# Kernel optimization log

Measured on AMD Instinct MI355X. Metric: run time of the kernel, lower is better.

## Reference

```python
import jax, jax.numpy as jnp
import numpy as np

EMBED_DIM = 384
HIDDEN_DIM = 512
CODEBOOK_SIZE = 256
NUM_QUANTIZERS = 4
COMMIT_WEIGHT = 0.25
BATCH = 65536


def setup_inputs() -> dict:
    key = jax.random.key(0)
    ks = jax.random.split(key, 10)
    s_in = 1.0 / np.sqrt(EMBED_DIM)
    s_h = 1.0 / np.sqrt(HIDDEN_DIM)
    return {
        "x": jax.random.normal(ks[0], (BATCH, EMBED_DIM), jnp.float32),
        "enc_w1": jax.random.uniform(ks[1], (EMBED_DIM, HIDDEN_DIM), jnp.float32, -s_in, s_in),
        "enc_b1": jnp.zeros((HIDDEN_DIM,), jnp.float32),
        "enc_w2": jax.random.uniform(ks[2], (HIDDEN_DIM, HIDDEN_DIM), jnp.float32, -s_h, s_h),
        "enc_b2": jnp.zeros((HIDDEN_DIM,), jnp.float32),
        "codebooks": jax.random.normal(ks[3], (NUM_QUANTIZERS, CODEBOOK_SIZE, HIDDEN_DIM), jnp.float32),
        "dec_w1": jax.random.uniform(ks[4], (HIDDEN_DIM, HIDDEN_DIM), jnp.float32, -s_h, s_h),
        "dec_b1": jnp.zeros((HIDDEN_DIM,), jnp.float32),
        "dec_w2": jax.random.uniform(ks[5], (HIDDEN_DIM, EMBED_DIM), jnp.float32, -s_h, s_h),
        "dec_b2": jnp.zeros((EMBED_DIM,), jnp.float32),
    }


def _residual_vq(z, codebooks):
    """Sequential residual VQ with straight-through estimator and commitment loss.
    z: [B, D]; codebooks: [Q, K, D]. Returns quantized [B, D], indices [B, Q], commit_loss scalar."""
    residual = z
    quantized_out = jnp.zeros_like(z)
    commit_loss = jnp.asarray(0.0, z.dtype)
    idx_list = []
    for q in range(NUM_QUANTIZERS):
        cb = codebooks[q]  # [K, D]
        # nearest code: argmin ||r - c||^2 == argmax (2 r.c - ||c||^2)
        scores = 2.0 * (residual @ cb.T) - jnp.sum(cb * cb, axis=-1)  # [B, K]
        idx = jnp.argmax(scores, axis=-1)  # [B]
        quant = cb[idx]  # [B, D] gather
        commit_loss = commit_loss + COMMIT_WEIGHT * jnp.mean(
            (residual - jax.lax.stop_gradient(quant)) ** 2)
        # straight-through: value = quant, gradient flows to residual
        quant_st = residual + jax.lax.stop_gradient(quant - residual)
        quantized_out = quantized_out + quant_st
        residual = residual - jax.lax.stop_gradient(quant)
        idx_list.append(idx)
    indices = jnp.stack(idx_list, axis=-1)  # [B, Q]
    return quantized_out, indices, commit_loss


def reference(x, enc_w1, enc_b1, enc_w2, enc_b2, codebooks,
              dec_w1, dec_b1, dec_w2, dec_b2):
    # encoder MLP
    z = jax.nn.relu(x @ enc_w1 + enc_b1) @ enc_w2 + enc_b2  # [B, H]
    quantized, indices, commit_loss = _residual_vq(z, codebooks)
    # decoder MLP
    recon = jax.nn.relu(quantized @ dec_w1 + dec_b1) @ dec_w2 + dec_b2  # [B, E]
    recon_loss = jnp.mean((recon - x) ** 2)
    return recon, indices, recon_loss, commit_loss
```

## Files before the change

kernel.cpp:

```cpp
#include <hip/hip_runtime.h>
#include <cfloat>
#include <cstddef>
#include <cstdint>


#define BATCH   65536
#define EDIM    384
#define HDIM    512
#define NCODE   256
#define NQ      4

#define OUT_IDX_OFF 25165824
#define OUT_RL_OFF  25427968
#define WS_P0       0
#define WS_P1       33554432
#define WS_CBSPL    67108864
#define WS_CNORM    67633152
#define WS_COMMITP  67634176
#define WS_RECONP   67636224
#define WS_W1S      67637760
#define WS_W2S      67834368
#define WS_W3S      68096512
#define WS_W4S      68358656

typedef _Float16 half8 __attribute__((ext_vector_type(8)));
typedef float    f32x16 __attribute__((ext_vector_type(16)));

__device__ __forceinline__ void cvt_hl8(const float* vs, half8& h, half8& l)
{
#pragma unroll
    for (int j = 0; j < 8; ++j) {
        _Float16 hv = (_Float16)vs[j];
        h[j] = hv;
        l[j] = (_Float16)(vs[j] - (float)hv);
    }
}

__device__ __forceinline__ void gll16(const unsigned short* g, unsigned short* l)
{
    __builtin_amdgcn_global_load_lds(
        (const __attribute__((address_space(1))) unsigned int*)g,
        (__attribute__((address_space(3))) unsigned int*)l, 16, 0, 0);
}

template <int N> __device__ __forceinline__ void waitvm()
{
    __builtin_amdgcn_sched_barrier(0);
    if constexpr (N == 0)      asm volatile("s_waitcnt vmcnt(0)" ::: "memory");
    else if constexpr (N == 4) asm volatile("s_waitcnt vmcnt(4)" ::: "memory");
    else if constexpr (N == 6) asm volatile("s_waitcnt vmcnt(6)" ::: "memory");
    __builtin_amdgcn_sched_barrier(0);
}
__device__ __forceinline__ void barrier_raw()
{
    __builtin_amdgcn_s_barrier();
    __builtin_amdgcn_sched_barrier(0);
}

__global__ __launch_bounds__(256)
void split_x(const float* __restrict__ x, unsigned short* __restrict__ xs)
{
    int u = blockIdx.x * 256 + threadIdx.x;
    int row = u / 48;
    int rem = u % 48;
    int kt = rem >> 1, khalf = rem & 1;
    const float* p = x + (size_t)row * EDIM + kt * 16 + khalf * 8;
    float vs[8];
#pragma unroll
    for (int j = 0; j < 8; ++j) vs[j] = p[j];
    half8 h, l;
    cvt_hl8(vs, h, l);
    unsigned short* o = xs + (size_t)row * 768 + kt * 32 + khalf * 8;
    *reinterpret_cast<half8*>(o)      = h;
    *reinterpret_cast<half8*>(o + 16) = l;
}

__global__ __launch_bounds__(256)
void split_w(const float* __restrict__ W, unsigned short* __restrict__ out,
             int N, int K)
{
    int u = blockIdx.x * 256 + threadIdx.x;
    int col  = u % N;
    int rem  = u / N;
    int khalf = rem & 1;
    int kt    = rem >> 1;
    int kbase = kt * 16 + khalf * 8;
    float vs[8];
#pragma unroll
    for (int j = 0; j < 8; ++j) vs[j] = W[(size_t)(kbase + j) * N + col];
    half8 h, l;
    cvt_hl8(vs, h, l);
    *reinterpret_cast<half8*>(out + ((size_t)(kt * 4 + khalf) * N + col) * 8)     = h;
    *reinterpret_cast<half8*>(out + ((size_t)(kt * 4 + 2 + khalf) * N + col) * 8) = l;
}

__global__ __launch_bounds__(256)
void split_cb(const float* __restrict__ cb, unsigned short* __restrict__ out)
{
    int u = blockIdx.x * 256 + threadIdx.x;
    int q    = u >> 14;
    int rem  = u & 16383;
    int code = rem >> 6;
    int kt   = (rem >> 1) & 31;
    int khalf = rem & 1;
    int k = kt * 16 + khalf * 8;
    const float* p = cb + ((size_t)(q * NCODE + code)) * HDIM + k;
    float vs[8];
#pragma unroll
    for (int j = 0; j < 8; ++j) vs[j] = p[j];
    half8 h, l;
    cvt_hl8(vs, h, l);
    size_t o = (size_t)(q * 32 + kt) * 8192 + (size_t)khalf * 2048 + (size_t)code * 8;
    *reinterpret_cast<half8*>(out + o)        = h;
    *reinterpret_cast<half8*>(out + o + 4096) = l;
}

__global__ __launch_bounds__(64)
void cnorm_kernel(const float* __restrict__ cb, float* __restrict__ cnorm)
{
    const int code = blockIdx.x;
    const int lane = threadIdx.x;
    const float* r = cb + (size_t)code * HDIM;
    float s = 0.f;
    for (int k = lane; k < HDIM; k += 64) s = fmaf(r[k], r[k], s);
#pragma unroll
    for (int off = 32; off > 0; off >>= 1) s += __shfl_down(s, off);
    if (lane == 0) cnorm[code] = s;
}

template <int BN, int NKT, int OMODE, bool RELU>
__global__ __launch_bounds__(256, 2)
void gemm_pl(const unsigned short* __restrict__ Ain,
             const unsigned short* __restrict__ Wsp,
             const float* __restrict__ bias, void* __restrict__ Cout,
             const float* __restrict__ X, float* __restrict__ lossP, int N)
{
    constexpr int WN  = BN / 128;
    constexpr int WM  = 4 / WN;
    constexpr int MR  = 128 / WM;
    constexpr int FM  = MR / 32;
    constexpr int K   = NKT * 16;
    constexpr int BOFF = 4096;
    constexpr int BUFU = 4096 + 4 * BN * 8;
    constexpr int NIB = BN / 64;
    constexpr int GPI = 2 + NIB;

    __shared__ __align__(16) unsigned short lds[3][BUFU];

    const int tid  = threadIdx.x;
    const int wid  = tid >> 6;
    const int lane = tid & 63;
    const int l31  = lane & 31;
    const int lh   = lane >> 5;
    const int wm   = wid / WN;
    const int wn   = wid % WN;
    const int row0 = blockIdx.y * 128;
    const int n0   = blockIdx.x * BN;

    f32x16 acc[FM][4];
#pragma unroll
    for (int m = 0; m < FM; ++m)
#pragma unroll
        for (int n = 0; n < 4; ++n) acc[m][n] = (f32x16)(0.0f);

    auto stageB = [&](int buf, int kt) {
        const unsigned short* img = Wsp + (size_t)kt * 4 * N * 8;
        unsigned short* dstb = &lds[buf][BOFF];
#pragma unroll
        for (int t = 0; t < NIB; ++t) {
            int e = (wid * NIB + t) * 64 + lane;
            int u = (BN == 256) ? (e >> 8) : (e >> 7);
            int c = e & (BN - 1);
            gll16(img + ((size_t)u * N + n0 + c) * 8, dstb + (size_t)e * 8);
        }
    };
    auto stageA = [&](int buf, int kt) {
#pragma unroll
        for (int t = 0; t < 2; ++t) {
            int i = wid * 2 + t;
            int u = i >> 1, rh = i & 1;
            int row = rh * 64 + lane;
            gll16(Ain + (size_t)(row0 + row) * (2 * K) + kt * 32 + u * 8,
                  &lds[buf][(size_t)i * 512 + (size_t)lane * 8]);
        }
    };
    auto compute = [&](int buf) {
        const unsigned short* Ab = &lds[buf][0];
        const unsigned short* Bb = &lds[buf][BOFF];
        half8 Ah[FM], Al[FM];
#pragma unroll
        for (int fm = 0; fm < FM; ++fm) {
            int row = wm * MR + fm * 32 + l31;
            Ah[fm] = *reinterpret_cast<const half8*>(Ab + (size_t)lh * 1024 + (size_t)row * 8);
            Al[fm] = *reinterpret_cast<const half8*>(Ab + (size_t)(2 + lh) * 1024 + (size_t)row * 8);
        }
#pragma unroll
        for (int nt = 0; nt < 4; ++nt) {
            int col = wn * 128 + nt * 32 + l31;
            half8 Bh = *reinterpret_cast<const half8*>(Bb + (size_t)lh * BN * 8 + (size_t)col * 8);
            half8 Bl = *reinterpret_cast<const half8*>(Bb + (size_t)(2 + lh) * BN * 8 + (size_t)col * 8);
#pragma unroll
            for (int fm = 0; fm < FM; ++fm) {
                acc[fm][nt] = __builtin_amdgcn_mfma_f32_32x32x16_f16(Ah[fm], Bh, acc[fm][nt], 0, 0, 0);
                acc[fm][nt] = __builtin_amdgcn_mfma_f32_32x32x16_f16(Ah[fm], Bl, acc[fm][nt], 0, 0, 0);
                acc[fm][nt] = __builtin_amdgcn_mfma_f32_32x32x16_f16(Al[fm], Bh, acc[fm][nt], 0, 0, 0);
            }
        }
    };

    stageA(0, 0); stageB(0, 0);
    stageA(1, 1); stageB(1, 1);
    waitvm<GPI>();
    barrier_raw();
    for (int kt = 0; kt < NKT; ++kt) {
        const int cur = kt % 3;
        if (kt + 2 < NKT) { const int nb = (kt + 2) % 3; stageA(nb, kt + 2); stageB(nb, kt + 2); }
        compute(cur);
        if (kt < NKT - 2) waitvm<GPI>(); else waitvm<0>();
        barrier_raw();
    }

    if constexpr (OMODE == 0) {
        unsigned short* o = (unsigned short*)Cout;
        const size_t rs = (size_t)N * 2;
#pragma unroll
        for (int fm = 0; fm < FM; ++fm) {
#pragma unroll
            for (int nt = 0; nt < 4; ++nt) {
                const int col = n0 + wn * 128 + nt * 32 + l31;
                const float b = bias[col];
                const size_t cbo = (size_t)(col >> 4) * 32 + (size_t)((col >> 3) & 1) * 8 + (col & 7);
#pragma unroll
                for (int rg = 0; rg < 16; ++rg) {
                    const int row = row0 + wm * MR + fm * 32 + (rg & 3) + 8 * (rg >> 2) + 4 * lh;
                    float v = acc[fm][nt][rg] + b;
                    if (RELU) v = v > 0.f ? v : 0.f;
                    _Float16 hv = (_Float16)v;
                    _Float16 lv = (_Float16)(v - (float)hv);
                    union { _Float16 f; unsigned short u; } ch, cl;
                    ch.f = hv; cl.f = lv;
                    o[(size_t)row * rs + cbo]      = ch.u;
                    o[(size_t)row * rs + cbo + 16] = cl.u;
                }
            }
        }
    } else {
        float* C = (float*)Cout;
        float lacc = 0.f;
#pragma unroll
        for (int fm = 0; fm < FM; ++fm) {
#pragma unroll
            for (int nt = 0; nt < 4; ++nt) {
                const int col = n0 + wn * 128 + nt * 32 + l31;
                const float b = bias[col];
#pragma unroll
                for (int rg = 0; rg < 16; ++rg) {
                    const int row = row0 + wm * MR + fm * 32 + (rg & 3) + 8 * (rg >> 2) + 4 * lh;
                    float v = acc[fm][nt][rg] + b;
                    if (RELU) v = v > 0.f ? v : 0.f;
                    C[(size_t)row * N + col] = v;
                    float d = v - X[(size_t)row * N + col];
                    lacc = fmaf(d, d, lacc);
                }
            }
        }
        __shared__ float red[256];
        red[tid] = lacc;
        __syncthreads();
        for (int s = 128; s > 0; s >>= 1) {
            if (tid < s) red[tid] += red[tid + s];
            __syncthreads();
        }
        if (tid == 0) lossP[blockIdx.y * gridDim.x + blockIdx.x] = red[0];
    }
}

template <bool LAST>
__global__ __launch_bounds__(256, 2)
void vq_stage(int q,
              const unsigned short* __restrict__ Rin, unsigned short* __restrict__ Rout,
              const unsigned short* __restrict__ zsrc,
              const unsigned short* __restrict__ cbs,
              const float* __restrict__ cb,
              const float* __restrict__ cnorm,
              float* __restrict__ idx_out,
              float* __restrict__ commitP)
{
    constexpr int NKT = 32;
    __shared__ __align__(16) unsigned short lds[3][12288];
    __shared__ float sval[2][128];
    __shared__ int   sidx[2][128];
    __shared__ int   idxbuf[128];
    __shared__ float red[256];

    const int tid  = threadIdx.x;
    const int wid  = tid >> 6;
    const int lane = tid & 63;
    const int l31  = lane & 31;
    const int lh   = lane >> 5;
    const int wm   = wid >> 1;
    const int wn   = wid & 1;
    const int row0 = blockIdx.x * 128;

    f32x16 acc[2][4];
#pragma unroll
    for (int m = 0; m < 2; ++m)
#pragma unroll
        for (int n = 0; n < 4; ++n) acc[m][n] = (f32x16)(0.0f);

    auto stageA = [&](int buf, int kt) {
#pragma unroll
        for (int t = 0; t < 2; ++t) {
            int i = wid * 2 + t;
            int u = i >> 1, rh = i & 1;
            int row = rh * 64 + lane;
            gll16(Rin + (size_t)(row0 + row) * 1024 + kt * 32 + u * 8,
                  &lds[buf][(size_t)i * 512 + (size_t)lane * 8]);
        }
    };
    auto stageB = [&](int buf, int kt) {
        const unsigned short* img = cbs + (size_t)(q * 32 + kt) * 8192;
        unsigned short* dstb = &lds[buf][4096];
#pragma unroll
        for (int t = 0; t < 4; ++t) {
            int e = (wid * 4 + t) * 64 + lane;
            gll16(img + (size_t)e * 8, dstb + (size_t)e * 8);
        }
    };
    auto compute = [&](int buf) {
        const unsigned short* Ab = &lds[buf][0];
        const unsigned short* Bb = &lds[buf][4096];
        half8 Ah[2], Al[2];
#pragma unroll
        for (int fm = 0; fm < 2; ++fm) {
            int row = wm * 64 + fm * 32 + l31;
            Ah[fm] = *reinterpret_cast<const half8*>(Ab + (size_t)lh * 1024 + (size_t)row * 8);
            Al[fm] = *reinterpret_cast<const half8*>(Ab + (size_t)(2 + lh) * 1024 + (size_t)row * 8);
        }
#pragma unroll
        for (int nt = 0; nt < 4; ++nt) {
            int col = wn * 128 + nt * 32 + l31;
            half8 Bh = *reinterpret_cast<const half8*>(Bb + (size_t)lh * 2048 + (size_t)col * 8);
            half8 Bl = *reinterpret_cast<const half8*>(Bb + (size_t)(2 + lh) * 2048 + (size_t)col * 8);
#pragma unroll
            for (int fm = 0; fm < 2; ++fm) {
                acc[fm][nt] = __builtin_amdgcn_mfma_f32_32x32x16_f16(Ah[fm], Bh, acc[fm][nt], 0, 0, 0);
                acc[fm][nt] = __builtin_amdgcn_mfma_f32_32x32x16_f16(Ah[fm], Bl, acc[fm][nt], 0, 0, 0);
                acc[fm][nt] = __builtin_amdgcn_mfma_f32_32x32x16_f16(Al[fm], Bh, acc[fm][nt], 0, 0, 0);
            }
        }
    };

    stageA(0, 0); stageB(0, 0);
    stageA(1, 1); stageB(1, 1);
    waitvm<6>();
    barrier_raw();
    for (int kt = 0; kt < NKT; ++kt) {
        const int cur = kt % 3;
        if (kt + 2 < NKT) { const int nb = (kt + 2) % 3; stageA(nb, kt + 2); stageB(nb, kt + 2); }
        compute(cur);
        if (kt < NKT - 2) waitvm<6>(); else waitvm<0>();
        barrier_raw();
    }

    const float* cn = cnorm + q * NCODE;
#pragma unroll
    for (int Mt = 0; Mt < 2; ++Mt) {
#pragma unroll
        for (int rg = 0; rg < 16; ++rg) {
            float bv = -FLT_MAX;
            int   bi = 0;
#pragma unroll
            for (int nt = 0; nt < 4; ++nt) {
                const int code = wn * 128 + nt * 32 + l31;
                float s = 2.f * acc[Mt][nt][rg] - cn[code];
                if (s > bv || (s == bv && code < bi)) { bv = s; bi = code; }
            }
#pragma unroll
            for (int m = 1; m < 32; m <<= 1) {
                float ov = __shfl_xor(bv, m, 64);
                int   oi = __shfl_xor(bi, m, 64);
                if (ov > bv || (ov == bv && oi < bi)) { bv = ov; bi = oi; }
            }
            if (l31 == 0) {
                int row = wm * 64 + Mt * 32 + (rg & 3) + 8 * (rg >> 2) + 4 * lh;
                sval[wn][row] = bv;
                sidx[wn][row] = bi;
            }
        }
    }
    __syncthreads();
    if (tid < 128) {
        float v0 = sval[0][tid], v1 = sval[1][tid];
        int   i0 = sidx[0][tid], i1 = sidx[1][tid];
        int b = (v1 > v0 || (v1 == v0 && i1 < i0)) ? i1 : i0;
        idxbuf[tid] = b;
        idx_out[(size_t)(row0 + tid) * NQ + q] = (float)b;
    }
    __syncthreads();

    float ca = 0.f;
    const int rgrp = tid >> 3;
    const int lpos = tid & 7;
#pragma unroll
    for (int rr = 0; rr < 4; ++rr) {
        const int row = rr * 32 + rgrp;
        const unsigned short* rip = Rin + (size_t)(row0 + row) * 1024;
        unsigned short*       rop = Rout + (size_t)(row0 + row) * 1024;
        const float* crow = cb + ((size_t)q * NCODE + idxbuf[row]) * HDIM;
        const unsigned short* zp = LAST ? (zsrc + (size_t)(row0 + row) * 1024) : nullptr;
#pragma unroll
        for (int j = 0; j < 8; ++j) {
            const int g = lpos + j * 8;
            const size_t off = (size_t)(g >> 1) * 32 + (size_t)(g & 1) * 8;
            half8 rh = *reinterpret_cast<const half8*>(rip + off);
            half8 rl = *reinterpret_cast<const half8*>(rip + off + 16);
            float4 c0 = *reinterpret_cast<const float4*>(crow + g * 8);
            float4 c1 = *reinterpret_cast<const float4*>(crow + g * 8 + 4);
            float cv[8] = {c0.x, c0.y, c0.z, c0.w, c1.x, c1.y, c1.z, c1.w};
            half8 zh, zl;
            if constexpr (LAST) {
                zh = *reinterpret_cast<const half8*>(zp + off);
                zl = *reinterpret_cast<const half8*>(zp + off + 16);
            }
            half8 oh, ol;
#pragma unroll
            for (int e = 0; e < 8; ++e) {
                float rv = (float)rh[e] + (float)rl[e];
                float d = rv - cv[e];
                ca = fmaf(d, d, ca);
                float ov = d;
                if constexpr (LAST) {
                    float zv = (float)zh[e] + (float)zl[e];
                    ov = zv - d;
                }
                _Float16 hv = (_Float16)ov;
                oh[e] = hv;
                ol[e] = (_Float16)(ov - (float)hv);
            }
            *reinterpret_cast<half8*>(rop + off)      = oh;
            *reinterpret_cast<half8*>(rop + off + 16) = ol;
        }
    }

    red[tid] = ca;
    __syncthreads();
    for (int s = 128; s > 0; s >>= 1) {
        if (tid < s) red[tid] += red[tid + s];
        __syncthreads();
    }
    if (tid == 0) commitP[q * 512 + blockIdx.x] = red[0];
}

__global__ __launch_bounds__(256)
void loss_reduce(const float* __restrict__ cP, int nc,
                 const float* __restrict__ rP, int nr,
                 float* __restrict__ out2)
{
    __shared__ float red[256];
    const int tid = threadIdx.x;

    float s = 0.f;
    for (int i = tid; i < nc; i += 256) s += cP[i];
    red[tid] = s;
    __syncthreads();
    for (int st = 128; st > 0; st >>= 1) {
        if (tid < st) red[tid] += red[tid + st];
        __syncthreads();
    }
    float ctot = red[0];
    __syncthreads();

    s = 0.f;
    for (int i = tid; i < nr; i += 256) s += rP[i];
    red[tid] = s;
    __syncthreads();
    for (int st = 128; st > 0; st >>= 1) {
        if (tid < st) red[tid] += red[tid + st];
        __syncthreads();
    }
    if (tid == 0) {
        out2[0] = red[0] / ((float)BATCH * (float)EDIM);
        out2[1] = 0.25f * ctot / ((float)BATCH * (float)HDIM);
    }
}

extern "C" void kernel_launch(void* const* d_in, const int* in_sizes, int n_in,
                              void* d_out, int out_size, void* d_ws, size_t ws_size,
                              hipStream_t stream)
{
    const float* x   = (const float*)d_in[0];
    const float* ew1 = (const float*)d_in[1];
    const float* eb1 = (const float*)d_in[2];
    const float* ew2 = (const float*)d_in[3];
    const float* eb2 = (const float*)d_in[4];
    const float* cb  = (const float*)d_in[5];
    const float* dw1 = (const float*)d_in[6];
    const float* db1 = (const float*)d_in[7];
    const float* dw2 = (const float*)d_in[8];
    const float* db2 = (const float*)d_in[9];

    float* out = (float*)d_out;
    float* ws  = (float*)d_ws;
    unsigned short* P0  = (unsigned short*)(ws + WS_P0);
    unsigned short* P1  = (unsigned short*)(ws + WS_P1);
    unsigned short* XS  = P1;
    unsigned short* cbs = (unsigned short*)(ws + WS_CBSPL);
    float* cn = ws + WS_CNORM;
    float* cP = ws + WS_COMMITP;
    float* rP = ws + WS_RECONP;
    unsigned short* w1s = (unsigned short*)(ws + WS_W1S);
    unsigned short* w2s = (unsigned short*)(ws + WS_W2S);
    unsigned short* w3s = (unsigned short*)(ws + WS_W3S);
    unsigned short* w4s = (unsigned short*)(ws + WS_W4S);

    cnorm_kernel<<<NQ * NCODE, 64, 0, stream>>>(cb, cn);
    split_cb<<<256, 256, 0, stream>>>(cb, cbs);
    split_x<<<BATCH * 48 / 256, 256, 0, stream>>>(x, XS);
    split_w<<<(EDIM / 16) * 2 * HDIM / 256, 256, 0, stream>>>(ew1, w1s, HDIM, EDIM);
    split_w<<<(HDIM / 16) * 2 * HDIM / 256, 256, 0, stream>>>(ew2, w2s, HDIM, HDIM);
    split_w<<<(HDIM / 16) * 2 * HDIM / 256, 256, 0, stream>>>(dw1, w3s, HDIM, HDIM);
    split_w<<<(HDIM / 16) * 2 * EDIM / 256, 256, 0, stream>>>(dw2, w4s, EDIM, HDIM);

    gemm_pl<256, 24, 0, true><<<dim3(HDIM / 256, BATCH / 128), 256, 0, stream>>>(
        XS, w1s, eb1, P0, nullptr, nullptr, HDIM);
    gemm_pl<256, 32, 0, false><<<dim3(HDIM / 256, BATCH / 128), 256, 0, stream>>>(
        P0, w2s, eb2, P1, nullptr, nullptr, HDIM);

    float* idxo = out + OUT_IDX_OFF;
    vq_stage<false><<<512, 256, 0, stream>>>(0, P1, P0, nullptr, cbs, cb, cn, idxo, cP);
    vq_stage<false><<<512, 256, 0, stream>>>(1, P0, P0, nullptr, cbs, cb, cn, idxo, cP);
    vq_stage<false><<<512, 256, 0, stream>>>(2, P0, P0, nullptr, cbs, cb, cn, idxo, cP);
    vq_stage<true ><<<512, 256, 0, stream>>>(3, P0, P1, P1,      cbs, cb, cn, idxo, cP);

    gemm_pl<256, 32, 0, true><<<dim3(HDIM / 256, BATCH / 128), 256, 0, stream>>>(
        P1, w3s, db1, P0, nullptr, nullptr, HDIM);
    gemm_pl<128, 32, 1, false><<<dim3(EDIM / 128, BATCH / 128), 256, 0, stream>>>(
        P0, w4s, db2, out, x, rP, EDIM);

    loss_reduce<<<1, 256, 0, stream>>>(cP, NQ * 512, rP,
                                       (BATCH / 128) * (EDIM / 128),
                                       out + OUT_RL_OFF);
}
```

Measured before the change: 989.6 us.

## Fuse four residual VQ stages into one kernel with LDS-resident residual

Replaces the four per-quantizer VQ launches with a single kernel. Each 512-thread block loads a 64-row residual tile (split fp16 hi/lo) into 128KB of LDS once, then runs all four quantizers in place. Only the final quantized output goes back to global memory. This removes the repeated global residual reads and writes and three kernel launches. In exchange, occupancy drops to one large block per CU, and codebook fragments are now read straight from global/L2 with no LDS staging, using half the row tile per codebook pass. That roughly doubles codebook traffic.

```diff
diff --git a/kernel.cpp b/kernel.cpp
--- a/kernel.cpp
+++ b/kernel.cpp
@@ -275,105 +275,75 @@
     }
 }
 
-template <bool LAST>
-__global__ __launch_bounds__(256, 2)
-void vq_stage(int q,
-              const unsigned short* __restrict__ Rin, unsigned short* __restrict__ Rout,
-              const unsigned short* __restrict__ zsrc,
+__global__ __launch_bounds__(512, 1)
+void vq_fused(const unsigned short* __restrict__ zs,
+              unsigned short* __restrict__ qout,
               const unsigned short* __restrict__ cbs,
               const float* __restrict__ cb,
               const float* __restrict__ cnorm,
               float* __restrict__ idx_out,
               float* __restrict__ commitP)
 {
-    constexpr int NKT = 32;
-    __shared__ __align__(16) unsigned short lds[3][12288];
-    __shared__ float sval[2][128];
-    __shared__ int   sidx[2][128];
-    __shared__ int   idxbuf[128];
-    __shared__ float red[256];
+    __shared__ __align__(16) unsigned short res[65536];
+    __shared__ float sval[4][64];
+    __shared__ int   sidx[4][64];
+    __shared__ int   idxbuf[64];
+    __shared__ float red[512];
 
     const int tid  = threadIdx.x;
     const int wid  = tid >> 6;
     const int lane = tid & 63;
     const int l31  = lane & 31;
     const int lh   = lane >> 5;
-    const int wm   = wid >> 1;
-    const int wn   = wid & 1;
-    const int row0 = blockIdx.x * 128;
-
-    f32x16 acc[2][4];
-#pragma unroll
-    for (int m = 0; m < 2; ++m)
-#pragma unroll
-        for (int n = 0; n < 4; ++n) acc[m][n] = (f32x16)(0.0f);
-
-    auto stageA = [&](int buf, int kt) {
-#pragma unroll
-        for (int t = 0; t < 2; ++t) {
-            int i = wid * 2 + t;
-            int u = i >> 1, rh = i & 1;
-            int row = rh * 64 + lane;
-            gll16(Rin + (size_t)(row0 + row) * 1024 + kt * 32 + u * 8,
-                  &lds[buf][(size_t)i * 512 + (size_t)lane * 8]);
-        }
-    };
-    auto stageB = [&](int buf, int kt) {
-        const unsigned short* img = cbs + (size_t)(q * 32 + kt) * 8192;
-        unsigned short* dstb = &lds[buf][4096];
-#pragma unroll
-        for (int t = 0; t < 4; ++t) {
-            int e = (wid * 4 + t) * 64 + lane;
-            gll16(img + (size_t)e * 8, dstb + (size_t)e * 8);
-        }
-    };
-    auto compute = [&](int buf) {
-        const unsigned short* Ab = &lds[buf][0];
-        const unsigned short* Bb = &lds[buf][4096];
-        half8 Ah[2], Al[2];
-#pragma unroll
-        for (int fm = 0; fm < 2; ++fm) {
-            int row = wm * 64 + fm * 32 + l31;
-            Ah[fm] = *reinterpret_cast<const half8*>(Ab + (size_t)lh * 1024 + (size_t)row * 8);
-            Al[fm] = *reinterpret_cast<const half8*>(Ab + (size_t)(2 + lh) * 1024 + (size_t)row * 8);
-        }
-#pragma unroll
-        for (int nt = 0; nt < 4; ++nt) {
-            int col = wn * 128 + nt * 32 + l31;
-            half8 Bh = *reinterpret_cast<const half8*>(Bb + (size_t)lh * 2048 + (size_t)col * 8);
-            half8 Bl = *reinterpret_cast<const half8*>(Bb + (size_t)(2 + lh) * 2048 + (size_t)col * 8);
-#pragma unroll
-            for (int fm = 0; fm < 2; ++fm) {
-                acc[fm][nt] = __builtin_amdgcn_mfma_f32_32x32x16_f16(Ah[fm], Bh, acc[fm][nt], 0, 0, 0);
-                acc[fm][nt] = __builtin_amdgcn_mfma_f32_32x32x16_f16(Ah[fm], Bl, acc[fm][nt], 0, 0, 0);
-                acc[fm][nt] = __builtin_amdgcn_mfma_f32_32x32x16_f16(Al[fm], Bh, acc[fm][nt], 0, 0, 0);
-            }
-        }
-    };
-
-    stageA(0, 0); stageB(0, 0);
-    stageA(1, 1); stageB(1, 1);
-    waitvm<6>();
-    barrier_raw();
-    for (int kt = 0; kt < NKT; ++kt) {
-        const int cur = kt % 3;
-        if (kt + 2 < NKT) { const int nb = (kt + 2) % 3; stageA(nb, kt + 2); stageB(nb, kt + 2); }
-        compute(cur);
-        if (kt < NKT - 2) waitvm<6>(); else waitvm<0>();
-        barrier_raw();
-    }
-
-    const float* cn = cnorm + q * NCODE;
-#pragma unroll
-    for (int Mt = 0; Mt < 2; ++Mt) {
+    const int wm   = wid >> 2;
+    const int wn   = wid & 3;
+    const int row0 = blockIdx.x * 64;
+
+#pragma unroll
+    for (int t = 0; t < 16; ++t) {
+        const int unit = wid * 16 + t;
+        const int kt = unit >> 2, u = unit & 3;
+        gll16(zs + (size_t)(row0 + lane) * 1024 + kt * 32 + u * 8,
+              res + (size_t)(kt * 4 + u) * 512 + (size_t)lane * 8);
+    }
+    __syncthreads();
+
+    const half8* c8 = reinterpret_cast<const half8*>(cbs);
+    float ca = 0.f;
+
+    for (int q = 0; q < NQ; ++q) {
+        const size_t qbase = (size_t)q * 32 * 1024;
+        const float* cn = cnorm + q * NCODE;
+
+        f32x16 acc[2];
+        acc[0] = (f32x16)(0.0f);
+        acc[1] = (f32x16)(0.0f);
+#pragma unroll
+        for (int kt = 0; kt < 32; ++kt) {
+            const unsigned short* Ab = res + (size_t)(kt * 4 + lh) * 512
+                                           + (size_t)(wm * 32 + l31) * 8;
+            half8 Ah = *reinterpret_cast<const half8*>(Ab);
+            half8 Al = *reinterpret_cast<const half8*>(Ab + 1024);
+            const size_t eh = qbase + (size_t)kt * 1024 + (size_t)lh * 256;
+#pragma unroll
+            for (int nt = 0; nt < 2; ++nt) {
+                const int code = wn * 64 + nt * 32 + l31;
+                half8 Bh = c8[eh + code];
+                half8 Bl = c8[eh + 512 + code];
+                acc[nt] = __builtin_amdgcn_mfma_f32_32x32x16_f16(Ah, Bh, acc[nt], 0, 0, 0);
+                acc[nt] = __builtin_amdgcn_mfma_f32_32x32x16_f16(Ah, Bl, acc[nt], 0, 0, 0);
+                acc[nt] = __builtin_amdgcn_mfma_f32_32x32x16_f16(Al, Bh, acc[nt], 0, 0, 0);
+            }
+        }
+
 #pragma unroll
         for (int rg = 0; rg < 16; ++rg) {
             float bv = -FLT_MAX;
             int   bi = 0;
 #pragma unroll
-            for (int nt = 0; nt < 4; ++nt) {
-                const int code = wn * 128 + nt * 32 + l31;
-                float s = 2.f * acc[Mt][nt][rg] - cn[code];
+            for (int nt = 0; nt < 2; ++nt) {
+                const int code = wn * 64 + nt * 32 + l31;
+                float s = 2.f * acc[nt][rg] - cn[code];
                 if (s > bv || (s == bv && code < bi)) { bv = s; bi = code; }
             }
 #pragma unroll
@@ -383,73 +353,77 @@
                 if (ov > bv || (ov == bv && oi < bi)) { bv = ov; bi = oi; }
             }
             if (l31 == 0) {
-                int row = wm * 64 + Mt * 32 + (rg & 3) + 8 * (rg >> 2) + 4 * lh;
+                const int row = wm * 32 + (rg & 3) + 8 * (rg >> 2) + 4 * lh;
                 sval[wn][row] = bv;
                 sidx[wn][row] = bi;
             }
         }
-    }
-    __syncthreads();
-    if (tid < 128) {
-        float v0 = sval[0][tid], v1 = sval[1][tid];
-        int   i0 = sidx[0][tid], i1 = sidx[1][tid];
-        int b = (v1 > v0 || (v1 == v0 && i1 < i0)) ? i1 : i0;
-        idxbuf[tid] = b;
-        idx_out[(size_t)(row0 + tid) * NQ + q] = (float)b;
-    }
-    __syncthreads();
-
-    float ca = 0.f;
-    const int rgrp = tid >> 3;
-    const int lpos = tid & 7;
-#pragma unroll
-    for (int rr = 0; rr < 4; ++rr) {
-        const int row = rr * 32 + rgrp;
-        const unsigned short* rip = Rin + (size_t)(row0 + row) * 1024;
-        unsigned short*       rop = Rout + (size_t)(row0 + row) * 1024;
-        const float* crow = cb + ((size_t)q * NCODE + idxbuf[row]) * HDIM;
-        const unsigned short* zp = LAST ? (zsrc + (size_t)(row0 + row) * 1024) : nullptr;
-#pragma unroll
-        for (int j = 0; j < 8; ++j) {
-            const int g = lpos + j * 8;
-            const size_t off = (size_t)(g >> 1) * 32 + (size_t)(g & 1) * 8;
-            half8 rh = *reinterpret_cast<const half8*>(rip + off);
-            half8 rl = *reinterpret_cast<const half8*>(rip + off + 16);
-            float4 c0 = *reinterpret_cast<const float4*>(crow + g * 8);
-            float4 c1 = *reinterpret_cast<const float4*>(crow + g * 8 + 4);
+        __syncthreads();
+        if (tid < 64) {
+            float bv = sval[0][tid];
+            int   bi = sidx[0][tid];
+#pragma unroll
+            for (int w = 1; w < 4; ++w) {
+                float v = sval[w][tid];
+                int   i = sidx[w][tid];
+                if (v > bv || (v == bv && i < bi)) { bv = v; bi = i; }
+            }
+            idxbuf[tid] = bi;
+            idx_out[(size_t)(row0 + tid) * NQ + q] = (float)bi;
+        }
+        __syncthreads();
+
+#pragma unroll
+        for (int t = 0; t < 8; ++t) {
+            const int pair = wid * 8 + t;
+            const int kt = pair >> 1, kh = pair & 1;
+            const size_t rb = (size_t)(kt * 4 + kh) * 512 + (size_t)lane * 8;
+            half8 rh = *reinterpret_cast<const half8*>(res + rb);
+            half8 rl = *reinterpret_cast<const half8*>(res + rb + 1024);
+            const float* crow = cb + ((size_t)(q * NCODE + idxbuf[lane])) * HDIM
+                                   + kt * 16 + kh * 8;
+            float4 c0 = *reinterpret_cast<const float4*>(crow);
+            float4 c1 = *reinterpret_cast<const float4*>(crow + 4);
             float cv[8] = {c0.x, c0.y, c0.z, c0.w, c1.x, c1.y, c1.z, c1.w};
-            half8 zh, zl;
-            if constexpr (LAST) {
-                zh = *reinterpret_cast<const half8*>(zp + off);
-                zl = *reinterpret_cast<const half8*>(zp + off + 16);
-            }
-            half8 oh, ol;
+            float d[8];
 #pragma unroll
             for (int e = 0; e < 8; ++e) {
                 float rv = (float)rh[e] + (float)rl[e];
-                float d = rv - cv[e];
-                ca = fmaf(d, d, ca);
-                float ov = d;
-                if constexpr (LAST) {
-                    float zv = (float)zh[e] + (float)zl[e];
-                    ov = zv - d;
-                }
-                _Float16 hv = (_Float16)ov;
-                oh[e] = hv;
-                ol[e] = (_Float16)(ov - (float)hv);
-            }
-            *reinterpret_cast<half8*>(rop + off)      = oh;
-            *reinterpret_cast<half8*>(rop + off + 16) = ol;
-        }
+                d[e] = rv - cv[e];
+                ca = fmaf(d[e], d[e], ca);
+            }
+            if (q < NQ - 1) {
+                half8 oh, ol;
+                cvt_hl8(d, oh, ol);
+                *reinterpret_cast<half8*>(res + rb)        = oh;
+                *reinterpret_cast<half8*>(res + rb + 1024) = ol;
+            } else {
+                const unsigned short* zp = zs + (size_t)(row0 + lane) * 1024
+                                              + kt * 32 + kh * 8;
+                half8 zh = *reinterpret_cast<const half8*>(zp);
+                half8 zl = *reinterpret_cast<const half8*>(zp + 16);
+                float qv[8];
+#pragma unroll
+                for (int e = 0; e < 8; ++e)
+                    qv[e] = ((float)zh[e] + (float)zl[e]) - d[e];
+                half8 oh, ol;
+                cvt_hl8(qv, oh, ol);
+                unsigned short* op = qout + (size_t)(row0 + lane) * 1024
+                                          + kt * 32 + kh * 8;
+                *reinterpret_cast<half8*>(op)      = oh;
+                *reinterpret_cast<half8*>(op + 16) = ol;
+            }
+        }
+        __syncthreads();
     }
 
     red[tid] = ca;
     __syncthreads();
-    for (int s = 128; s > 0; s >>= 1) {
+    for (int s = 256; s > 0; s >>= 1) {
         if (tid < s) red[tid] += red[tid + s];
         __syncthreads();
     }
-    if (tid == 0) commitP[q * 512 + blockIdx.x] = red[0];
+    if (tid == 0) commitP[blockIdx.x] = red[0];
 }
 
 __global__ __launch_bounds__(256)
@@ -528,17 +502,14 @@
         P0, w2s, eb2, P1, nullptr, nullptr, HDIM);
 
     float* idxo = out + OUT_IDX_OFF;
-    vq_stage<false><<<512, 256, 0, stream>>>(0, P1, P0, nullptr, cbs, cb, cn, idxo, cP);
-    vq_stage<false><<<512, 256, 0, stream>>>(1, P0, P0, nullptr, cbs, cb, cn, idxo, cP);
-    vq_stage<false><<<512, 256, 0, stream>>>(2, P0, P0, nullptr, cbs, cb, cn, idxo, cP);
-    vq_stage<true ><<<512, 256, 0, stream>>>(3, P0, P1, P1,      cbs, cb, cn, idxo, cP);
+    vq_fused<<<BATCH / 64, 512, 0, stream>>>(P1, P0, cbs, cb, cn, idxo, cP);
 
     gemm_pl<256, 32, 0, true><<<dim3(HDIM / 256, BATCH / 128), 256, 0, stream>>>(
-        P1, w3s, db1, P0, nullptr, nullptr, HDIM);
+        P0, w3s, db1, P1, nullptr, nullptr, HDIM);
     gemm_pl<128, 32, 1, false><<<dim3(EDIM / 128, BATCH / 128), 256, 0, stream>>>(
-        P0, w4s, db2, out, x, rP, EDIM);
-
-    loss_reduce<<<1, 256, 0, stream>>>(cP, NQ * 512, rP,
+        P1, w4s, db2, out, x, rP, EDIM);
+
+    loss_reduce<<<1, 256, 0, stream>>>(cP, BATCH / 64, rP,
                                        (BATCH / 128) * (EDIM / 128),
                                        out + OUT_RL_OFF);
 }
```

Result: slower. 1.155 ms (+16.7%).

## Reformulate residual VQ via precomputed codebook cross-Gram corrections

Applied to the files above, without the earlier changes.

Each VQ stage now scores the original encoder output z against its codebook and subtracts precomputed codebook-pair dot products (a 6-pair Gram table) for the codes already chosen. This removes the materialization of residuals between stages. A single gather kernel then sums the four selected codes into the quantized output. The commitment loss is rebuilt from row norms and the best scores, which adds small extra GEMMs and a rownorm pass and may change floating-point rounding versus explicit residual subtraction.

```diff
diff --git a/kernel.cpp b/kernel.cpp
--- a/kernel.cpp
+++ b/kernel.cpp
@@ -14,7 +14,7 @@
 #define OUT_RL_OFF  25427968
 #define WS_P0       0
 #define WS_P1       33554432
-#define WS_CBSPL    67108864
+#define WS_CBW      67108864
 #define WS_CNORM    67633152
 #define WS_COMMITP  67634176
 #define WS_RECONP   67636224
@@ -22,6 +22,11 @@
 #define WS_W2S      67834368
 #define WS_W3S      68096512
 #define WS_W4S      68358656
+#define WS_CBA      68555264
+#define WS_G6       69079552
+#define WS_ZN       69472768
+#define WS_SSTAR    69538304
+#define WS_IDXI     69800448
 
 typedef _Float16 half8 __attribute__((ext_vector_type(8)));
 typedef float    f32x16 __attribute__((ext_vector_type(16)));
@@ -47,7 +52,6 @@
 {
     __builtin_amdgcn_sched_barrier(0);
     if constexpr (N == 0)      asm volatile("s_waitcnt vmcnt(0)" ::: "memory");
-    else if constexpr (N == 4) asm volatile("s_waitcnt vmcnt(4)" ::: "memory");
     else if constexpr (N == 6) asm volatile("s_waitcnt vmcnt(6)" ::: "memory");
     __builtin_amdgcn_sched_barrier(0);
 }
@@ -58,19 +62,21 @@
 }
 
 __global__ __launch_bounds__(256)
-void split_x(const float* __restrict__ x, unsigned short* __restrict__ xs)
+void split_act(const float* __restrict__ src, unsigned short* __restrict__ dst,
+               int K)
 {
     int u = blockIdx.x * 256 + threadIdx.x;
-    int row = u / 48;
-    int rem = u % 48;
-    int kt = rem >> 1, khalf = rem & 1;
-    const float* p = x + (size_t)row * EDIM + kt * 16 + khalf * 8;
+    int upr = K >> 3;
+    int row = u / upr;
+    int rem = u % upr;
+    int kt = rem >> 1, kh = rem & 1;
+    const float* p = src + (size_t)row * K + kt * 16 + kh * 8;
     float vs[8];
 #pragma unroll
     for (int j = 0; j < 8; ++j) vs[j] = p[j];
     half8 h, l;
     cvt_hl8(vs, h, l);
-    unsigned short* o = xs + (size_t)row * 768 + kt * 32 + khalf * 8;
+    unsigned short* o = dst + (size_t)row * (2 * K) + kt * 32 + kh * 8;
     *reinterpret_cast<half8*>(o)      = h;
     *reinterpret_cast<half8*>(o + 16) = l;
 }
@@ -95,24 +101,21 @@
 }
 
 __global__ __launch_bounds__(256)
-void split_cb(const float* __restrict__ cb, unsigned short* __restrict__ out)
+void split_cbw(const float* __restrict__ cb, unsigned short* __restrict__ out)
 {
     int u = blockIdx.x * 256 + threadIdx.x;
-    int q    = u >> 14;
-    int rem  = u & 16383;
-    int code = rem >> 6;
-    int kt   = (rem >> 1) & 31;
-    int khalf = rem & 1;
-    int k = kt * 16 + khalf * 8;
-    const float* p = cb + ((size_t)(q * NCODE + code)) * HDIM + k;
+    int col = u & 1023;
+    int rem = u >> 10;
+    int kh = rem & 1;
+    int kt = rem >> 1;
+    const float* p = cb + (size_t)col * HDIM + kt * 16 + kh * 8;
     float vs[8];
 #pragma unroll
     for (int j = 0; j < 8; ++j) vs[j] = p[j];
     half8 h, l;
     cvt_hl8(vs, h, l);
-    size_t o = (size_t)(q * 32 + kt) * 8192 + (size_t)khalf * 2048 + (size_t)code * 8;
-    *reinterpret_cast<half8*>(out + o)        = h;
-    *reinterpret_cast<half8*>(out + o + 4096) = l;
+    *reinterpret_cast<half8*>(out + ((size_t)(kt * 4 + kh) * 1024 + col) * 8)     = h;
+    *reinterpret_cast<half8*>(out + ((size_t)(kt * 4 + 2 + kh) * 1024 + col) * 8) = l;
 }
 
 __global__ __launch_bounds__(64)
@@ -126,6 +129,26 @@
 #pragma unroll
     for (int off = 32; off > 0; off >>= 1) s += __shfl_down(s, off);
     if (lane == 0) cnorm[code] = s;
+}
+
+__global__ __launch_bounds__(256)
+void rownorm(const unsigned short* __restrict__ zs, float* __restrict__ zn)
+{
+    const int tid = threadIdx.x, wid = tid >> 6, lane = tid & 63;
+    const int row = blockIdx.x * 4 + wid;
+    const unsigned short* p = zs + (size_t)row * 1024
+                                 + (lane >> 1) * 32 + (lane & 1) * 8;
+    half8 h = *reinterpret_cast<const half8*>(p);
+    half8 l = *reinterpret_cast<const half8*>(p + 16);
+    float s = 0.f;
+#pragma unroll
+    for (int e = 0; e < 8; ++e) {
+        float v = (float)h[e] + (float)l[e];
+        s = fmaf(v, v, s);
+    }
+#pragma unroll
+    for (int off = 32; off > 0; off >>= 1) s += __shfl_down(s, off);
+    if (lane == 0) zn[row] = s;
 }
 
 template <int BN, int NKT, int OMODE, bool RELU>
@@ -143,7 +166,6 @@
     constexpr int BOFF = 4096;
     constexpr int BUFU = 4096 + 4 * BN * 8;
     constexpr int NIB = BN / 64;
-    constexpr int GPI = 2 + NIB;
 
     __shared__ __align__(16) unsigned short lds[3][BUFU];
 
@@ -210,13 +232,13 @@
 
     stageA(0, 0); stageB(0, 0);
     stageA(1, 1); stageB(1, 1);
-    waitvm<GPI>();
+    waitvm<6>();
     barrier_raw();
     for (int kt = 0; kt < NKT; ++kt) {
         const int cur = kt % 3;
         if (kt + 2 < NKT) { const int nb = (kt + 2) % 3; stageA(nb, kt + 2); stageB(nb, kt + 2); }
         compute(cur);
-        if (kt < NKT - 2) waitvm<GPI>(); else waitvm<0>();
+        if (kt < NKT - 2) waitvm<6>(); else waitvm<0>();
         barrier_raw();
     }
 
@@ -244,7 +266,7 @@
                 }
             }
         }
-    } else {
+    } else if constexpr (OMODE == 1) {
         float* C = (float*)Cout;
         float lacc = 0.f;
 #pragma unroll
@@ -272,26 +294,38 @@
             __syncthreads();
         }
         if (tid == 0) lossP[blockIdx.y * gridDim.x + blockIdx.x] = red[0];
-    }
-}
-
-template <bool LAST>
+    } else {
+        float* C = (float*)Cout;
+#pragma unroll
+        for (int fm = 0; fm < FM; ++fm) {
+#pragma unroll
+            for (int nt = 0; nt < 4; ++nt) {
+                const int col = wn * 128 + nt * 32 + l31;
+#pragma unroll
+                for (int rg = 0; rg < 16; ++rg) {
+                    const int row = row0 + wm * MR + fm * 32 + (rg & 3) + 8 * (rg >> 2) + 4 * lh;
+                    C[(size_t)row * 256 + col] = acc[fm][nt][rg];
+                }
+            }
+        }
+    }
+}
+
+template <int Q>
 __global__ __launch_bounds__(256, 2)
-void vq_stage(int q,
-              const unsigned short* __restrict__ Rin, unsigned short* __restrict__ Rout,
-              const unsigned short* __restrict__ zsrc,
-              const unsigned short* __restrict__ cbs,
-              const float* __restrict__ cb,
+void vq_score(const unsigned short* __restrict__ zs,
+              const unsigned short* __restrict__ cbw,
+              const float* __restrict__ G6,
               const float* __restrict__ cnorm,
               float* __restrict__ idx_out,
-              float* __restrict__ commitP)
+              int* __restrict__ idxi,
+              float* __restrict__ sstar)
 {
     constexpr int NKT = 32;
+    constexpr int N   = 1024;
     __shared__ __align__(16) unsigned short lds[3][12288];
     __shared__ float sval[2][128];
     __shared__ int   sidx[2][128];
-    __shared__ int   idxbuf[128];
-    __shared__ float red[256];
 
     const int tid  = threadIdx.x;
     const int wid  = tid >> 6;
@@ -301,6 +335,7 @@
     const int wm   = wid >> 1;
     const int wn   = wid & 1;
     const int row0 = blockIdx.x * 128;
+    const int n0   = Q * 256;
 
     f32x16 acc[2][4];
 #pragma unroll
@@ -308,23 +343,25 @@
 #pragma unroll
         for (int n = 0; n < 4; ++n) acc[m][n] = (f32x16)(0.0f);
 
+    auto stageB = [&](int buf, int kt) {
+        const unsigned short* img = cbw + (size_t)kt * 4 * N * 8;
+        unsigned short* dstb = &lds[buf][4096];
+#pragma unroll
+        for (int t = 0; t < 4; ++t) {
+            int e = (wid * 4 + t) * 64 + lane;
+            int u = e >> 8;
+            int c = e & 255;
+            gll16(img + ((size_t)u * N + n0 + c) * 8, dstb + (size_t)e * 8);
+        }
+    };
     auto stageA = [&](int buf, int kt) {
 #pragma unroll
         for (int t = 0; t < 2; ++t) {
             int i = wid * 2 + t;
             int u = i >> 1, rh = i & 1;
             int row = rh * 64 + lane;
-            gll16(Rin + (size_t)(row0 + row) * 1024 + kt * 32 + u * 8,
+            gll16(zs + (size_t)(row0 + row) * 1024 + kt * 32 + u * 8,
                   &lds[buf][(size_t)i * 512 + (size_t)lane * 8]);
-        }
-    };
-    auto stageB = [&](int buf, int kt) {
-        const unsigned short* img = cbs + (size_t)(q * 32 + kt) * 8192;
-        unsigned short* dstb = &lds[buf][4096];
-#pragma unroll
-        for (int t = 0; t < 4; ++t) {
-            int e = (wid * 4 + t) * 64 + lane;
-            gll16(img + (size_t)e * 8, dstb + (size_t)e * 8);
         }
     };
     auto compute = [&](int buf) {
@@ -363,17 +400,29 @@
         barrier_raw();
     }
 
-    const float* cn = cnorm + q * NCODE;
-#pragma unroll
-    for (int Mt = 0; Mt < 2; ++Mt) {
+    const float* cn = cnorm + Q * NCODE;
+    constexpr int PAIR0 = (Q == 1) ? 0 : (Q == 2) ? 1 : 2;
+    constexpr int PAIR1 = (Q == 2) ? 3 : 4;
+    constexpr int PAIR2 = 5;
+#pragma unroll
+    for (int fm = 0; fm < 2; ++fm) {
 #pragma unroll
         for (int rg = 0; rg < 16; ++rg) {
+            const int grow = row0 + wm * 64 + fm * 32 + (rg & 3) + 8 * (rg >> 2) + 4 * lh;
+            const float* gr0 = nullptr; const float* gr1 = nullptr; const float* gr2 = nullptr;
+            if constexpr (Q > 0) gr0 = G6 + ((size_t)PAIR0 * 256 + idxi[0 * 65536 + grow]) * 256;
+            if constexpr (Q > 1) gr1 = G6 + ((size_t)PAIR1 * 256 + idxi[1 * 65536 + grow]) * 256;
+            if constexpr (Q > 2) gr2 = G6 + ((size_t)PAIR2 * 256 + idxi[2 * 65536 + grow]) * 256;
             float bv = -FLT_MAX;
             int   bi = 0;
 #pragma unroll
             for (int nt = 0; nt < 4; ++nt) {
                 const int code = wn * 128 + nt * 32 + l31;
-                float s = 2.f * acc[Mt][nt][rg] - cn[code];
+                float a = acc[fm][nt][rg];
+                if constexpr (Q > 0) a -= gr0[code];
+                if constexpr (Q > 1) a -= gr1[code];
+                if constexpr (Q > 2) a -= gr2[code];
+                float s = 2.f * a - cn[code];
                 if (s > bv || (s == bv && code < bi)) { bv = s; bi = code; }
             }
 #pragma unroll
@@ -383,7 +432,7 @@
                 if (ov > bv || (ov == bv && oi < bi)) { bv = ov; bi = oi; }
             }
             if (l31 == 0) {
-                int row = wm * 64 + Mt * 32 + (rg & 3) + 8 * (rg >> 2) + 4 * lh;
+                const int row = wm * 64 + fm * 32 + (rg & 3) + 8 * (rg >> 2) + 4 * lh;
                 sval[wn][row] = bv;
                 sidx[wn][row] = bi;
             }
@@ -393,53 +442,60 @@
     if (tid < 128) {
         float v0 = sval[0][tid], v1 = sval[1][tid];
         int   i0 = sidx[0][tid], i1 = sidx[1][tid];
-        int b = (v1 > v0 || (v1 == v0 && i1 < i0)) ? i1 : i0;
-        idxbuf[tid] = b;
-        idx_out[(size_t)(row0 + tid) * NQ + q] = (float)b;
-    }
-    __syncthreads();
-
+        float bv = (v1 > v0 || (v1 == v0 && i1 < i0)) ? v1 : v0;
+        int   bi = (v1 > v0 || (v1 == v0 && i1 < i0)) ? i1 : i0;
+        const int grow = row0 + tid;
+        idxi[Q * 65536 + grow]  = bi;
+        sstar[Q * 65536 + grow] = bv;
+        idx_out[(size_t)grow * NQ + Q] = (float)bi;
+    }
+}
+
+__global__ __launch_bounds__(256)
+void vq_quant(const int* __restrict__ idxi, const float* __restrict__ sstar,
+              const float* __restrict__ zn, const float* __restrict__ cb,
+              unsigned short* __restrict__ qout, float* __restrict__ commitP)
+{
+    __shared__ float red[256];
+    const int tid = threadIdx.x, wid = tid >> 6, lane = tid & 63;
     float ca = 0.f;
-    const int rgrp = tid >> 3;
-    const int lpos = tid & 7;
-#pragma unroll
-    for (int rr = 0; rr < 4; ++rr) {
-        const int row = rr * 32 + rgrp;
-        const unsigned short* rip = Rin + (size_t)(row0 + row) * 1024;
-        unsigned short*       rop = Rout + (size_t)(row0 + row) * 1024;
-        const float* crow = cb + ((size_t)q * NCODE + idxbuf[row]) * HDIM;
-        const unsigned short* zp = LAST ? (zsrc + (size_t)(row0 + row) * 1024) : nullptr;
-#pragma unroll
-        for (int j = 0; j < 8; ++j) {
-            const int g = lpos + j * 8;
-            const size_t off = (size_t)(g >> 1) * 32 + (size_t)(g & 1) * 8;
-            half8 rh = *reinterpret_cast<const half8*>(rip + off);
-            half8 rl = *reinterpret_cast<const half8*>(rip + off + 16);
-            float4 c0 = *reinterpret_cast<const float4*>(crow + g * 8);
-            float4 c1 = *reinterpret_cast<const float4*>(crow + g * 8 + 4);
-            float cv[8] = {c0.x, c0.y, c0.z, c0.w, c1.x, c1.y, c1.z, c1.w};
-            half8 zh, zl;
-            if constexpr (LAST) {
-                zh = *reinterpret_cast<const half8*>(zp + off);
-                zl = *reinterpret_cast<const half8*>(zp + off + 16);
-            }
-            half8 oh, ol;
-#pragma unroll
-            for (int e = 0; e < 8; ++e) {
-                float rv = (float)rh[e] + (float)rl[e];
-                float d = rv - cv[e];
-                ca = fmaf(d, d, ca);
-                float ov = d;
-                if constexpr (LAST) {
-                    float zv = (float)zh[e] + (float)zl[e];
-                    ov = zv - d;
-                }
-                _Float16 hv = (_Float16)ov;
-                oh[e] = hv;
-                ol[e] = (_Float16)(ov - (float)hv);
-            }
-            *reinterpret_cast<half8*>(rop + off)      = oh;
-            *reinterpret_cast<half8*>(rop + off + 16) = ol;
+
+#pragma unroll
+    for (int t = 0; t < 8; ++t) {
+        const int row = blockIdx.x * 32 + wid * 8 + t;
+        const int i0 = idxi[row],          i1 = idxi[65536 + row];
+        const int i2 = idxi[131072 + row], i3 = idxi[196608 + row];
+        const int koff = lane * 8;
+        const float* c0 = cb + ((size_t)(0 * NCODE + i0)) * HDIM + koff;
+        const float* c1 = cb + ((size_t)(1 * NCODE + i1)) * HDIM + koff;
+        const float* c2 = cb + ((size_t)(2 * NCODE + i2)) * HDIM + koff;
+        const float* c3 = cb + ((size_t)(3 * NCODE + i3)) * HDIM + koff;
+        float q[8];
+#pragma unroll
+        for (int half = 0; half < 2; ++half) {
+            float4 v0 = *reinterpret_cast<const float4*>(c0 + half * 4);
+            float4 v1 = *reinterpret_cast<const float4*>(c1 + half * 4);
+            float4 v2 = *reinterpret_cast<const float4*>(c2 + half * 4);
+            float4 v3 = *reinterpret_cast<const float4*>(c3 + half * 4);
+            q[half * 4 + 0] = ((v0.x + v1.x) + v2.x) + v3.x;
+            q[half * 4 + 1] = ((v0.y + v1.y) + v2.y) + v3.y;
+            q[half * 4 + 2] = ((v0.z + v1.z) + v2.z) + v3.z;
+            q[half * 4 + 3] = ((v0.w + v1.w) + v2.w) + v3.w;
+        }
+        half8 oh, ol;
+        cvt_hl8(q, oh, ol);
+        unsigned short* op = qout + (size_t)row * 1024
+                                  + (lane >> 1) * 32 + (lane & 1) * 8;
+        *reinterpret_cast<half8*>(op)      = oh;
+        *reinterpret_cast<half8*>(op + 16) = ol;
+
+        if (lane == 0) {
+            float rn = zn[row];
+            rn -= sstar[row];           float cm = rn;
+            rn -= sstar[65536 + row];   cm += rn;
+            rn -= sstar[131072 + row];  cm += rn;
+            rn -= sstar[196608 + row];  cm += rn;
+            ca += cm;
         }
     }
 
@@ -449,7 +505,7 @@
         if (tid < s) red[tid] += red[tid + s];
         __syncthreads();
     }
-    if (tid == 0) commitP[q * 512 + blockIdx.x] = red[0];
+    if (tid == 0) commitP[blockIdx.x] = red[0];
 }
 
 __global__ __launch_bounds__(256)
@@ -505,7 +561,12 @@
     unsigned short* P0  = (unsigned short*)(ws + WS_P0);
     unsigned short* P1  = (unsigned short*)(ws + WS_P1);
     unsigned short* XS  = P1;
-    unsigned short* cbs = (unsigned short*)(ws + WS_CBSPL);
+    unsigned short* cbw = (unsigned short*)(ws + WS_CBW);
+    unsigned short* cba = (unsigned short*)(ws + WS_CBA);
+    float* G6 = ws + WS_G6;
+    float* zn = ws + WS_ZN;
+    float* ss = ws + WS_SSTAR;
+    int*   ii = (int*)(ws + WS_IDXI);
     float* cn = ws + WS_CNORM;
     float* cP = ws + WS_COMMITP;
     float* rP = ws + WS_RECONP;
@@ -515,30 +576,45 @@
     unsigned short* w4s = (unsigned short*)(ws + WS_W4S);
 
     cnorm_kernel<<<NQ * NCODE, 64, 0, stream>>>(cb, cn);
-    split_cb<<<256, 256, 0, stream>>>(cb, cbs);
-    split_x<<<BATCH * 48 / 256, 256, 0, stream>>>(x, XS);
+    split_act<<<BATCH * 48 / 256, 256, 0, stream>>>(x, XS, EDIM);
+    split_act<<<1024 * 64 / 256, 256, 0, stream>>>(cb, cba, HDIM);
+    split_cbw<<<256, 256, 0, stream>>>(cb, cbw);
     split_w<<<(EDIM / 16) * 2 * HDIM / 256, 256, 0, stream>>>(ew1, w1s, HDIM, EDIM);
     split_w<<<(HDIM / 16) * 2 * HDIM / 256, 256, 0, stream>>>(ew2, w2s, HDIM, HDIM);
     split_w<<<(HDIM / 16) * 2 * HDIM / 256, 256, 0, stream>>>(dw1, w3s, HDIM, HDIM);
     split_w<<<(HDIM / 16) * 2 * EDIM / 256, 256, 0, stream>>>(dw2, w4s, EDIM, HDIM);
 
+    {
+        const int pairs[6][2] = {{0,1},{0,2},{0,3},{1,2},{1,3},{2,3}};
+        for (int pi = 0; pi < 6; ++pi) {
+            const int p = pairs[pi][0], q = pairs[pi][1];
+            gemm_pl<256, 32, 2, false><<<dim3(1, 2), 256, 0, stream>>>(
+                cba + (size_t)p * 256 * 1024, cbw + (size_t)q * 256 * 8,
+                nullptr, G6 + (size_t)pi * 65536, nullptr, nullptr, 1024);
+        }
+    }
+
     gemm_pl<256, 24, 0, true><<<dim3(HDIM / 256, BATCH / 128), 256, 0, stream>>>(
         XS, w1s, eb1, P0, nullptr, nullptr, HDIM);
     gemm_pl<256, 32, 0, false><<<dim3(HDIM / 256, BATCH / 128), 256, 0, stream>>>(
         P0, w2s, eb2, P1, nullptr, nullptr, HDIM);
 
+    rownorm<<<BATCH / 4, 256, 0, stream>>>(P1, zn);
+
     float* idxo = out + OUT_IDX_OFF;
-    vq_stage<false><<<512, 256, 0, stream>>>(0, P1, P0, nullptr, cbs, cb, cn, idxo, cP);
-    vq_stage<false><<<512, 256, 0, stream>>>(1, P0, P0, nullptr, cbs, cb, cn, idxo, cP);
-    vq_stage<false><<<512, 256, 0, stream>>>(2, P0, P0, nullptr, cbs, cb, cn, idxo, cP);
-    vq_stage<true ><<<512, 256, 0, stream>>>(3, P0, P1, P1,      cbs, cb, cn, idxo, cP);
+    vq_score<0><<<BATCH / 128, 256, 0, stream>>>(P1, cbw, G6, cn, idxo, ii, ss);
+    vq_score<1><<<BATCH / 128, 256, 0, stream>>>(P1, cbw, G6, cn, idxo, ii, ss);
+    vq_score<2><<<BATCH / 128, 256, 0, stream>>>(P1, cbw, G6, cn, idxo, ii, ss);
+    vq_score<3><<<BATCH / 128, 256, 0, stream>>>(P1, cbw, G6, cn, idxo, ii, ss);
+
+    vq_quant<<<BATCH / 32, 256, 0, stream>>>(ii, ss, zn, cb, P0, cP);
 
     gemm_pl<256, 32, 0, true><<<dim3(HDIM / 256, BATCH / 128), 256, 0, stream>>>(
-        P1, w3s, db1, P0, nullptr, nullptr, HDIM);
+        P0, w3s, db1, P1, nullptr, nullptr, HDIM);
     gemm_pl<128, 32, 1, false><<<dim3(EDIM / 128, BATCH / 128), 256, 0, stream>>>(
-        P0, w4s, db2, out, x, rP, EDIM);
-
-    loss_reduce<<<1, 256, 0, stream>>>(cP, NQ * 512, rP,
+        P1, w4s, db2, out, x, rP, EDIM);
+
+    loss_reduce<<<1, 256, 0, stream>>>(cP, BATCH / 32, rP,
                                        (BATCH / 128) * (EDIM / 128),
                                        out + OUT_RL_OFF);
 }
```

After: 996.1 us. No clear change (+0.7%).
